# Kernel optimization log

Hardware: AMD Instinct MI355X
Metric: run time of the kernel (lower is better)

The kernel has to match this reference:

```python
import jax, jax.numpy as jnp
import numpy as np

DECAY = 0.4  # from x_f + 0.6*y_{f-1} + 3 - y_{f-1} == x_f - 0.4*y_{f-1} + 3
BIAS = 3.0


def setup_inputs() -> dict:
    key = jax.random.key(0)
    x = jax.random.normal(key, (8, 16, 3, 224, 224), dtype=jnp.float32)
    return {"x": x}


def reference(x) -> jnp.ndarray:
    # Faithful translation of Temporal.forward, including the aliasing /
    # repeated-zeroing semantics of rgb_differ (traced from the source):
    #   - batch 0:   y[0]=x[0];  y[f] = x[f] - 0.4*y[f-1] + 3   (data recurrence)
    #   - batches 1..b-2: all zeros (re-zeroed by each later outer iteration)
    #   - batch b-1: z[0]=0;     z[f] = 3 - 0.4*z[f-1]          (scalar recurrence,
    #                 broadcast over c,h,w; input-independent)
    # then permute(0,1,4,3,2): [b,t,c,h,w] -> [b,t,w,h,c].
    b, t = x.shape[0], x.shape[1]

    # batch-0 data-dependent recurrence over time via scan (elementwise in c,h,w)
    def step(carry, xt):
        y = xt - DECAY * carry + BIAS
        return y, y

    y0_first = x[0, 0]                                   # [c,h,w]
    _, y0_rest = jax.lax.scan(step, y0_first, x[0, 1:])  # [t-1,c,h,w]
    y0 = jnp.concatenate([y0_first[None], y0_rest], axis=0)  # [t,c,h,w]

    out = jnp.zeros_like(x).at[0].set(y0)

    if b > 1:
        # last-batch input-independent scalar recurrence, broadcast spatially
        def zstep(c, _):
            z = BIAS - DECAY * c
            return z, z

        _, z_rest = jax.lax.scan(zstep, jnp.float32(0.0), None, length=t - 1)
        z = jnp.concatenate([jnp.zeros((1,), x.dtype), z_rest.astype(x.dtype)])  # [t]
        out = out.at[-1].set(jnp.broadcast_to(z[:, None, None, None], x.shape[1:]))

    return jnp.transpose(out, (0, 1, 4, 3, 2))  # [b,t,w,h,c]
```

## Files before the change

### kernel.cpp

```cpp
#include <hip/hip_runtime.h>


#define SP        150528
#define TT        16
#define CH_STRIDE 50176
#define BSTRIDE   2408448

#define NWT    7
#define NTILES 196

#define FILL4   4214784
#define TSLICE4 37632
#define NBLOCKS 2048
#define NFILL   (NBLOCKS - NTILES)
#define RFILL   2276
#define SPREAD  9

__global__ __launch_bounds__(256) void temporal_fused(
    const float* __restrict__ x, float* __restrict__ out)
{
    const int tid = threadIdx.x;
    const int bid = blockIdx.x;

    const bool is_tile = (bid % SPREAD == 0) && (bid / SPREAD) < NTILES;

    if (is_tile) {
        const int tileid = bid / SPREAD;
        const int h0 = (tileid / NWT) * 8;
        const int w0 = (tileid % NWT) * 32;
        const int dw = tid & 31;
        const int hh = tid >> 5;
        const int rbase = (h0 + hh) * 224 + w0 + dw;

        float v[TT][3];
        #pragma unroll
        for (int t = 0; t < TT; ++t) {
            #pragma unroll
            for (int c = 0; c < 3; ++c)
                v[t][c] = x[t * SP + c * CH_STRIDE + rbase];
        }

        const int ob = (w0 + dw) * 672 + (h0 + hh) * 3;
        float y0 = v[0][0], y1 = v[0][1], y2 = v[0][2];
        out[ob + 0] = y0;
        out[ob + 1] = y1;
        out[ob + 2] = y2;
        #pragma unroll
        for (int t = 1; t < TT; ++t) {
            y0 = v[t][0] - 0.4f * y0 + 3.0f;
            y1 = v[t][1] - 0.4f * y1 + 3.0f;
            y2 = v[t][2] - 0.4f * y2 + 3.0f;
            const int o = t * SP + ob;
            out[o + 0] = y0;
            out[o + 1] = y1;
            out[o + 2] = y2;
        }
        return;
    }

    const int tiles_before = min((bid + SPREAD - 1) / SPREAD, NTILES);
    const int fidx = bid - tiles_before;

    float4* out4 = reinterpret_cast<float4*>(out + BSTRIDE);
    int q   = fidx * RFILL;
    int end = q + RFILL;
    if (end > FILL4) end = FILL4;

    while (q < end) {
        const int slice = q / TSLICE4;
        int send = (slice + 1) * TSLICE4;
        if (send > end) send = end;
        float zv = 0.0f;
        if ((slice >> 4) == 6) {
            const int t = slice & 15;
            float z = 0.0f;
            for (int i = 0; i < t; ++i) z = 3.0f - 0.4f * z;
            zv = z;
        }
        const float4 val = make_float4(zv, zv, zv, zv);
        for (int i = q + tid; i < send; i += 256)
            out4[i] = val;
        q = send;
    }
}

extern "C" void kernel_launch(void* const* d_in, const int* in_sizes, int n_in,
                              void* d_out, int out_size, void* d_ws, size_t ws_size,
                              hipStream_t stream) {
    const float* x = (const float*)d_in[0];
    float* out = (float*)d_out;
    temporal_fused<<<NBLOCKS, 256, 0, stream>>>(x, out);
}
```

Baseline: 17.84 us.

## Stage transposed tile outputs in LDS for coalesced vector nontemporal stores

The recurrence tiles now write their results into a swizzled shared-memory buffer, then read them back as 16-byte vectors and write contiguous output rows, instead of scattering three strided scalar stores per thread per timestep. The fill path also switches its zero/constant stores to nontemporal vector stores. This targets uncoalesced global writes caused by the [c,h,w]->[w,h,c] transpose, at the cost of 48KB LDS per block (which is also allocated for the fill blocks and may limit occupancy) and a block barrier.

```diff
diff --git a/kernel.cpp b/kernel.cpp
--- a/kernel.cpp
+++ b/kernel.cpp
@@ -1,5 +1,7 @@
 #include <hip/hip_runtime.h>
 
+
+typedef float fx4 __attribute__((ext_vector_type(4)));
 
 #define SP        150528
 #define TT        16
@@ -22,6 +24,8 @@
     const int tid = threadIdx.x;
     const int bid = blockIdx.x;
 
+    __shared__ float lds[TT * 32 * 24];
+
     const bool is_tile = (bid % SPREAD == 0) && (bid / SPREAD) < NTILES;
 
     if (is_tile) {
@@ -40,20 +44,42 @@
                 v[t][c] = x[t * SP + c * CH_STRIDE + rbase];
         }
 
-        const int ob = (w0 + dw) * 672 + (h0 + hh) * 3;
+        int wbase[3];
+        #pragma unroll
+        for (int c = 0; c < 3; ++c) {
+            const int idx = hh * 3 + c;
+            const int s = idx >> 2, o = idx & 3;
+            wbase[c] = dw * 24 + ((s + dw) % 6) * 4 + o;
+        }
+
         float y0 = v[0][0], y1 = v[0][1], y2 = v[0][2];
-        out[ob + 0] = y0;
-        out[ob + 1] = y1;
-        out[ob + 2] = y2;
         #pragma unroll
-        for (int t = 1; t < TT; ++t) {
-            y0 = v[t][0] - 0.4f * y0 + 3.0f;
-            y1 = v[t][1] - 0.4f * y1 + 3.0f;
-            y2 = v[t][2] - 0.4f * y2 + 3.0f;
-            const int o = t * SP + ob;
-            out[o + 0] = y0;
-            out[o + 1] = y1;
-            out[o + 2] = y2;
+        for (int t = 0; t < TT; ++t) {
+            if (t > 0) {
+                y0 = v[t][0] - 0.4f * y0 + 3.0f;
+                y1 = v[t][1] - 0.4f * y1 + 3.0f;
+                y2 = v[t][2] - 0.4f * y2 + 3.0f;
+            }
+            lds[t * 768 + wbase[0]] = y0;
+            lds[t * 768 + wbase[1]] = y1;
+            lds[t * 768 + wbase[2]] = y2;
+        }
+        __syncthreads();
+
+        const fx4* lds4 = reinterpret_cast<const fx4*>(lds);
+        const int ob0 = w0 * 672 + h0 * 3;
+        #pragma unroll
+        for (int k = 0; k < 12; ++k) {
+            const int j = tid + k * 256;
+            const int t = j / 192;
+            const int r = j - t * 192;
+            const int w = r / 6;
+            const int piece = r - w * 6;
+            const int phys = (piece + w) % 6;
+            const fx4 f4 = lds4[(t * 768 + w * 24 + phys * 4) >> 2];
+            fx4* dst = reinterpret_cast<fx4*>(
+                out + t * SP + ob0 + w * 672 + piece * 4);
+            __builtin_nontemporal_store(f4, dst);
         }
         return;
     }
@@ -61,7 +87,7 @@
     const int tiles_before = min((bid + SPREAD - 1) / SPREAD, NTILES);
     const int fidx = bid - tiles_before;
 
-    float4* out4 = reinterpret_cast<float4*>(out + BSTRIDE);
+    fx4* out4 = reinterpret_cast<fx4*>(out + BSTRIDE);
     int q   = fidx * RFILL;
     int end = q + RFILL;
     if (end > FILL4) end = FILL4;
@@ -77,9 +103,10 @@
             for (int i = 0; i < t; ++i) z = 3.0f - 0.4f * z;
             zv = z;
         }
-        const float4 val = make_float4(zv, zv, zv, zv);
+        fx4 val;
+        val.x = zv; val.y = zv; val.z = zv; val.w = zv;
         for (int i = q + tid; i < send; i += 256)
-            out4[i] = val;
+            __builtin_nontemporal_store(val, &out4[i]);
         q = send;
     }
 }
```

Result: slower. 24.48 us (+37.3%).
